# Kernel optimization log

Measured on AMD Instinct MI355X. Metric: run time of the kernel, lower is better.

Reference implementation:

```python
import jax, jax.numpy as jnp
import numpy as np

N_NODES = 50000
N_EDGES = 800000
D_IN, D_HID, D_OUT = 128, 256, 128


def _glorot(key, shape):
    fan_in, fan_out = shape[1], shape[0]
    lim = (6.0 / (fan_in + fan_out)) ** 0.5
    return jax.random.uniform(key, shape, jnp.float32, -lim, lim)


def setup_inputs() -> dict:
    key = jax.random.key(0)
    ks = jax.random.split(key, 8)
    x = jax.random.normal(ks[0], (N_NODES, D_IN), dtype=jnp.float32)
    edge_index = jax.random.randint(ks[1], (2, N_EDGES), 0, N_NODES, dtype=jnp.int64)
    # Layer 1: SAGEConv(D_IN -> D_HID); Layer 2: SAGEConv(D_HID -> D_OUT)
    # PyG SAGEConv: out = lin_l(mean_aggr(x_j)) + lin_r(x); bias lives in lin_l.
    Wl1 = _glorot(ks[2], (D_HID, D_IN))
    bl1 = jnp.zeros((D_HID,), jnp.float32)
    Wr1 = _glorot(ks[3], (D_HID, D_IN))
    Wl2 = _glorot(ks[4], (D_OUT, D_HID))
    bl2 = jnp.zeros((D_OUT,), jnp.float32)
    Wr2 = _glorot(ks[5], (D_OUT, D_HID))
    return {"x": x, "Wl1": Wl1, "bl1": bl1, "Wr1": Wr1,
            "Wl2": Wl2, "bl2": bl2, "Wr2": Wr2, "edge_index": edge_index}


def _sage_conv(x, src, dst, deg_inv, Wl, bl, Wr):
    # gather source features per edge, sum into dst buckets, normalize by in-degree
    msg_sum = jax.ops.segment_sum(x[src], dst, num_segments=N_NODES)  # [N, d_in]
    mean = msg_sum * deg_inv  # mean aggregation; isolated nodes -> zeros
    return mean @ Wl.T + bl + x @ Wr.T


def reference(x, Wl1, bl1, Wr1, Wl2, bl2, Wr2, edge_index):
    src, dst = edge_index[0], edge_index[1]
    deg = jax.ops.segment_sum(jnp.ones((N_EDGES,), jnp.float32), dst,
                              num_segments=N_NODES)
    deg_inv = (1.0 / jnp.maximum(deg, 1.0))[:, None]  # [N, 1]
    h = _sage_conv(x, src, dst, deg_inv, Wl1, bl1, Wr1)
    h = jax.nn.relu(h)  # dropout is identity in eval mode
    out = _sage_conv(h, src, dst, deg_inv, Wl2, bl2, Wr2)
    return out
```

## Files before the change

### kernel.cpp

```cpp
#include <hip/hip_runtime.h>
#include <hip/hip_fp16.h>

#define N_NODES 50000
#define N_EDGES 800000
#define D_IN 128
#define D_HID 256
#define D_OUT 128
#define NCHUNK 196
#define GEMM_GRID 512

typedef _Float16 f16x8 __attribute__((ext_vector_type(8)));
typedef float f32x4 __attribute__((ext_vector_type(4)));


__global__ void zero_deg(int* __restrict__ deg) {
    int i = blockIdx.x * blockDim.x + threadIdx.x;
    if (i < N_NODES) deg[i] = 0;
}

__global__ void deg_rank_kernel(const int* __restrict__ dst, int* __restrict__ deg,
                                int* __restrict__ rank) {
    int i = blockIdx.x * blockDim.x + threadIdx.x;
    if (i < N_EDGES) rank[i] = atomicAdd(&deg[dst[i]], 1);
}

__global__ void chunk_sum(const int* __restrict__ deg, int* __restrict__ partial) {
    __shared__ int s[256];
    int i = blockIdx.x * 256 + threadIdx.x;
    s[threadIdx.x] = (i < N_NODES) ? deg[i] : 0;
    __syncthreads();
    for (int off = 128; off > 0; off >>= 1) {
        if (threadIdx.x < off) s[threadIdx.x] += s[threadIdx.x + off];
        __syncthreads();
    }
    if (threadIdx.x == 0) partial[blockIdx.x] = s[0];
}

__global__ void chunk_scan(const int* __restrict__ partial, int* __restrict__ chunkOff) {
    __shared__ int s[256];
    int tid = threadIdx.x;
    int v = (tid < NCHUNK) ? partial[tid] : 0;
    s[tid] = v;
    __syncthreads();
    for (int off = 1; off < 256; off <<= 1) {
        int t = (tid >= off) ? s[tid - off] : 0;
        __syncthreads();
        s[tid] += t;
        __syncthreads();
    }
    if (tid < NCHUNK) chunkOff[tid] = s[tid] - v;
}

__global__ void scatter_scan(const int* __restrict__ deg, const int* __restrict__ chunkOff,
                             int* __restrict__ row_ptr, float* __restrict__ deg_inv) {
    __shared__ int s[256];
    int tid = threadIdx.x;
    int i = blockIdx.x * 256 + tid;
    int v = (i < N_NODES) ? deg[i] : 0;
    s[tid] = v;
    __syncthreads();
    for (int off = 1; off < 256; off <<= 1) {
        int t = (tid >= off) ? s[tid - off] : 0;
        __syncthreads();
        s[tid] += t;
        __syncthreads();
    }
    if (i < N_NODES) {
        int rp = chunkOff[blockIdx.x] + s[tid] - v;
        row_ptr[i] = rp;
        deg_inv[i] = 1.0f / fmaxf((float)v, 1.0f);
        if (i == N_NODES - 1) row_ptr[N_NODES] = N_EDGES;
    }
}

__global__ void fill_csr(const int* __restrict__ src, const int* __restrict__ dst,
                         const int* __restrict__ rank, const int* __restrict__ row_ptr,
                         int* __restrict__ csr_src) {
    int e = blockIdx.x * blockDim.x + threadIdx.x;
    if (e < N_EDGES) {
        csr_src[row_ptr[dst[e]] + rank[e]] = src[e];
    }
}


__global__ void cvt_half(const float* __restrict__ in, __half2* __restrict__ out, int n2) {
    int i = blockIdx.x * blockDim.x + threadIdx.x;
    if (i < n2) {
        float2 v = ((const float2*)in)[i];
        out[i] = __float22half2_rn(v);
    }
}

__global__ void cvt_weights(const float* __restrict__ a, const float* __restrict__ b,
                            const float* __restrict__ c, const float* __restrict__ d,
                            __half2* __restrict__ oa, __half2* __restrict__ ob,
                            __half2* __restrict__ oc, __half2* __restrict__ od) {
    int i = blockIdx.x * 256 + threadIdx.x;
    if (i < 16384) {
        oa[i] = __float22half2_rn(((const float2*)a)[i]);
        ob[i] = __float22half2_rn(((const float2*)b)[i]);
        oc[i] = __float22half2_rn(((const float2*)c)[i]);
        od[i] = __float22half2_rn(((const float2*)d)[i]);
    }
}


__global__ __launch_bounds__(256)
void gather_mean_h(const __half2* __restrict__ feat, const int* __restrict__ row_ptr,
                   const int* __restrict__ csr_src, const float* __restrict__ deg_inv,
                   __half2* __restrict__ outv) {
    const int lane = threadIdx.x & 63;
    const int n = blockIdx.x * 4 + (threadIdx.x >> 6);
    const int beg = row_ptr[n];
    const int end = row_ptr[n + 1];
    float a0 = 0.f, a1 = 0.f;
    int e = beg;
    for (; e + 8 <= end; e += 8) {
        int s0 = csr_src[e + 0], s1 = csr_src[e + 1];
        int s2 = csr_src[e + 2], s3 = csr_src[e + 3];
        int s4 = csr_src[e + 4], s5 = csr_src[e + 5];
        int s6 = csr_src[e + 6], s7 = csr_src[e + 7];
        float2 v0 = __half22float2(feat[s0 * 64 + lane]);
        float2 v1 = __half22float2(feat[s1 * 64 + lane]);
        float2 v2 = __half22float2(feat[s2 * 64 + lane]);
        float2 v3 = __half22float2(feat[s3 * 64 + lane]);
        float2 v4 = __half22float2(feat[s4 * 64 + lane]);
        float2 v5 = __half22float2(feat[s5 * 64 + lane]);
        float2 v6 = __half22float2(feat[s6 * 64 + lane]);
        float2 v7 = __half22float2(feat[s7 * 64 + lane]);
        a0 += ((v0.x + v1.x) + (v2.x + v3.x)) + ((v4.x + v5.x) + (v6.x + v7.x));
        a1 += ((v0.y + v1.y) + (v2.y + v3.y)) + ((v4.y + v5.y) + (v6.y + v7.y));
    }
    for (; e + 4 <= end; e += 4) {
        int s0 = csr_src[e + 0], s1 = csr_src[e + 1];
        int s2 = csr_src[e + 2], s3 = csr_src[e + 3];
        float2 v0 = __half22float2(feat[s0 * 64 + lane]);
        float2 v1 = __half22float2(feat[s1 * 64 + lane]);
        float2 v2 = __half22float2(feat[s2 * 64 + lane]);
        float2 v3 = __half22float2(feat[s3 * 64 + lane]);
        a0 += (v0.x + v1.x) + (v2.x + v3.x);
        a1 += (v0.y + v1.y) + (v2.y + v3.y);
    }
    for (; e < end; ++e) {
        float2 v = __half22float2(feat[csr_src[e] * 64 + lane]);
        a0 += v.x;
        a1 += v.y;
    }
    float di = deg_inv[n];
    outv[n * 64 + lane] = __float22half2_rn(make_float2(a0 * di, a1 * di));
}

__global__ __launch_bounds__(256)
void gather_mean_add_f32(const __half2* __restrict__ feat, const int* __restrict__ row_ptr,
                         const int* __restrict__ csr_src, const float* __restrict__ deg_inv,
                         float* __restrict__ out) {
    const int lane = threadIdx.x & 63;
    const int n = blockIdx.x * 4 + (threadIdx.x >> 6);
    const int beg = row_ptr[n];
    const int end = row_ptr[n + 1];
    float a0 = 0.f, a1 = 0.f;
    int e = beg;
    for (; e + 8 <= end; e += 8) {
        int s0 = csr_src[e + 0], s1 = csr_src[e + 1];
        int s2 = csr_src[e + 2], s3 = csr_src[e + 3];
        int s4 = csr_src[e + 4], s5 = csr_src[e + 5];
        int s6 = csr_src[e + 6], s7 = csr_src[e + 7];
        float2 v0 = __half22float2(feat[s0 * 64 + lane]);
        float2 v1 = __half22float2(feat[s1 * 64 + lane]);
        float2 v2 = __half22float2(feat[s2 * 64 + lane]);
        float2 v3 = __half22float2(feat[s3 * 64 + lane]);
        float2 v4 = __half22float2(feat[s4 * 64 + lane]);
        float2 v5 = __half22float2(feat[s5 * 64 + lane]);
        float2 v6 = __half22float2(feat[s6 * 64 + lane]);
        float2 v7 = __half22float2(feat[s7 * 64 + lane]);
        a0 += ((v0.x + v1.x) + (v2.x + v3.x)) + ((v4.x + v5.x) + (v6.x + v7.x));
        a1 += ((v0.y + v1.y) + (v2.y + v3.y)) + ((v4.y + v5.y) + (v6.y + v7.y));
    }
    for (; e + 4 <= end; e += 4) {
        int s0 = csr_src[e + 0], s1 = csr_src[e + 1];
        int s2 = csr_src[e + 2], s3 = csr_src[e + 3];
        float2 v0 = __half22float2(feat[s0 * 64 + lane]);
        float2 v1 = __half22float2(feat[s1 * 64 + lane]);
        float2 v2 = __half22float2(feat[s2 * 64 + lane]);
        float2 v3 = __half22float2(feat[s3 * 64 + lane]);
        a0 += (v0.x + v1.x) + (v2.x + v3.x);
        a1 += (v0.y + v1.y) + (v2.y + v3.y);
    }
    for (; e < end; ++e) {
        float2 v = __half22float2(feat[csr_src[e] * 64 + lane]);
        a0 += v.x;
        a1 += v.y;
    }
    float di = deg_inv[n];
    float2* o = (float2*)(out + (size_t)n * 128) + lane;
    float2 v = *o;
    v.x += a0 * di;
    v.y += a1 * di;
    *o = v;
}


__global__ __launch_bounds__(256, 2)
void gemm_l1(const __half* __restrict__ Aa, const __half* __restrict__ Ba,
             const __half* __restrict__ Ab, const __half* __restrict__ Bb,
             const float* __restrict__ bias, __half* __restrict__ H) {
    const int lane = threadIdx.x & 63;
    const int wave = threadIdx.x >> 6;
    const int quad = lane >> 4;
    const int l16 = lane & 15;
    const int koff = quad * 8;

    f16x8 bf[2][4][4];
    #pragma unroll
    for (int p = 0; p < 2; ++p) {
        const __half* __restrict__ B = p ? Bb : Ba;
        #pragma unroll
        for (int kc = 0; kc < 4; ++kc)
            #pragma unroll
            for (int nt = 0; nt < 4; ++nt)
                bf[p][kc][nt] = *(const f16x8*)(
                    B + (size_t)(wave * 64 + nt * 16 + l16) * D_IN + kc * 32 + koff);
    }
    float bv[4];
    #pragma unroll
    for (int nt = 0; nt < 4; ++nt) bv[nt] = bias[wave * 64 + nt * 16 + l16];

    const int NT = N_NODES / 16;
    const int g = gridDim.x;

    auto loadA = [&](int t, f16x8 (&a)[2][4]) {
        const size_t arow = (size_t)(t * 16 + l16) * D_IN + koff;
        #pragma unroll
        for (int kc = 0; kc < 4; ++kc) {
            a[0][kc] = *(const f16x8*)(Aa + arow + kc * 32);
            a[1][kc] = *(const f16x8*)(Ab + arow + kc * 32);
        }
    };
    auto step = [&](int tile, const f16x8 (&a)[2][4]) {
        f32x4 acc[4] = {};
        #pragma unroll
        for (int p = 0; p < 2; ++p)
            #pragma unroll
            for (int kc = 0; kc < 4; ++kc)
                #pragma unroll
                for (int nt = 0; nt < 4; ++nt)
                    acc[nt] = __builtin_amdgcn_mfma_f32_16x16x32_f16(
                        a[p][kc], bf[p][kc][nt], acc[nt], 0, 0, 0);
        #pragma unroll
        for (int nt = 0; nt < 4; ++nt) {
            int col = wave * 64 + nt * 16 + l16;
            #pragma unroll
            for (int r = 0; r < 4; ++r) {
                int row = tile * 16 + quad * 4 + r;
                H[(size_t)row * D_HID + col] =
                    __float2half(fmaxf(acc[nt][r] + bv[nt], 0.f));
            }
        }
    };

    f16x8 A0[2][4], A1[2][4];
    int tile = blockIdx.x;
    loadA(tile, A0);
    while (true) {
        if (tile + g < NT) loadA(tile + g, A1);
        step(tile, A0);
        tile += g;
        if (tile >= NT) break;
        if (tile + g < NT) loadA(tile + g, A0);
        step(tile, A1);
        tile += g;
        if (tile >= NT) break;
    }
}

__global__ __launch_bounds__(256, 2)
void gemm_l2(const __half* __restrict__ Hh, const __half* __restrict__ B0,
             const __half* __restrict__ B1, const float* __restrict__ bias,
             __half* __restrict__ P, float* __restrict__ out) {
    const int lane = threadIdx.x & 63;
    const int wave = threadIdx.x >> 6;
    const int quad = lane >> 4;
    const int l16 = lane & 15;
    const int koff = quad * 8;

    f16x8 bf0[8][2], bf1[8][2];
    #pragma unroll
    for (int kc = 0; kc < 8; ++kc)
        #pragma unroll
        for (int nt = 0; nt < 2; ++nt) {
            size_t brow = (size_t)(wave * 32 + nt * 16 + l16) * D_HID + kc * 32 + koff;
            bf0[kc][nt] = *(const f16x8*)(B0 + brow);
            bf1[kc][nt] = *(const f16x8*)(B1 + brow);
        }
    float bv[2];
    #pragma unroll
    for (int nt = 0; nt < 2; ++nt) bv[nt] = bias[wave * 32 + nt * 16 + l16];

    const int NT = N_NODES / 16;
    const int g = gridDim.x;

    auto loadA = [&](int t, f16x8 (&a)[8]) {
        const size_t arow = (size_t)(t * 16 + l16) * D_HID + koff;
        #pragma unroll
        for (int kc = 0; kc < 8; ++kc)
            a[kc] = *(const f16x8*)(Hh + arow + kc * 32);
    };
    auto step = [&](int tile, const f16x8 (&a)[8]) {
        f32x4 acc0[2] = {};
        f32x4 acc1[2] = {};
        #pragma unroll
        for (int kc = 0; kc < 8; ++kc)
            #pragma unroll
            for (int nt = 0; nt < 2; ++nt) {
                acc0[nt] = __builtin_amdgcn_mfma_f32_16x16x32_f16(
                    a[kc], bf0[kc][nt], acc0[nt], 0, 0, 0);
                acc1[nt] = __builtin_amdgcn_mfma_f32_16x16x32_f16(
                    a[kc], bf1[kc][nt], acc1[nt], 0, 0, 0);
            }
        #pragma unroll
        for (int nt = 0; nt < 2; ++nt) {
            int col = wave * 32 + nt * 16 + l16;
            #pragma unroll
            for (int r = 0; r < 4; ++r) {
                int row = tile * 16 + quad * 4 + r;
                P[(size_t)row * D_OUT + col] = __float2half(acc0[nt][r]);
                out[(size_t)row * D_OUT + col] = acc1[nt][r] + bv[nt];
            }
        }
    };

    f16x8 A0[8], A1[8];
    int tile = blockIdx.x;
    loadA(tile, A0);
    while (true) {
        if (tile + g < NT) loadA(tile + g, A1);
        step(tile, A0);
        tile += g;
        if (tile >= NT) break;
        if (tile + g < NT) loadA(tile + g, A0);
        step(tile, A1);
        tile += g;
        if (tile >= NT) break;
    }
}

extern "C" void kernel_launch(void* const* d_in, const int* in_sizes, int n_in,
                              void* d_out, int out_size, void* d_ws, size_t ws_size,
                              hipStream_t stream) {
    const float* x   = (const float*)d_in[0];
    const float* Wl1 = (const float*)d_in[1];
    const float* bl1 = (const float*)d_in[2];
    const float* Wr1 = (const float*)d_in[3];
    const float* Wl2 = (const float*)d_in[4];
    const float* bl2 = (const float*)d_in[5];
    const float* Wr2 = (const float*)d_in[6];
    const int*   ei  = (const int*)d_in[7];
    const int* src = ei;
    const int* dst = ei + N_EDGES;
    float* out = (float*)d_out;

    char* w = (char*)d_ws;
    auto alloc = [&](size_t bytes) {
        char* r = w;
        w += (bytes + 255) & ~(size_t)255;
        return r;
    };
    int*     deg       = (int*)alloc((size_t)N_NODES * 4);
    int*     row_ptr   = (int*)alloc((size_t)(N_NODES + 1) * 4);
    int*     rank      = (int*)alloc((size_t)N_EDGES * 4);
    int*     partial   = (int*)alloc(NCHUNK * 4);
    int*     chunkOff  = (int*)alloc(NCHUNK * 4);
    int*     csr_src   = (int*)alloc((size_t)N_EDGES * 4);
    float*   deg_inv   = (float*)alloc((size_t)N_NODES * 4);
    __half2* xb        = (__half2*)alloc((size_t)N_NODES * 64 * 4);
    __half2* mean1     = (__half2*)alloc((size_t)N_NODES * 64 * 4);
    __half*  h         = (__half*)alloc((size_t)N_NODES * 256 * 2);
    __half2* pb        = (__half2*)alloc((size_t)N_NODES * 64 * 4);
    __half*  wl1h      = (__half*)alloc(4 * 32768 * 2);
    __half*  wr1h = wl1h + 32768;
    __half*  wl2h = wr1h + 32768;
    __half*  wr2h = wl2h + 32768;

    zero_deg<<<(N_NODES + 255) / 256, 256, 0, stream>>>(deg);
    deg_rank_kernel<<<(N_EDGES + 255) / 256, 256, 0, stream>>>(dst, deg, rank);
    chunk_sum<<<NCHUNK, 256, 0, stream>>>(deg, partial);
    chunk_scan<<<1, 256, 0, stream>>>(partial, chunkOff);
    scatter_scan<<<NCHUNK, 256, 0, stream>>>(deg, chunkOff, row_ptr, deg_inv);
    fill_csr<<<(N_EDGES + 255) / 256, 256, 0, stream>>>(src, dst, rank, row_ptr, csr_src);

    cvt_half<<<12500, 256, 0, stream>>>(x, xb, N_NODES * 64);
    cvt_weights<<<64, 256, 0, stream>>>(Wl1, Wr1, Wl2, Wr2,
        (__half2*)wl1h, (__half2*)wr1h, (__half2*)wl2h, (__half2*)wr2h);

    gather_mean_h<<<12500, 256, 0, stream>>>(xb, row_ptr, csr_src, deg_inv, mean1);
    gemm_l1<<<GEMM_GRID, 256, 0, stream>>>(
        (const __half*)mean1, wl1h, (const __half*)xb, wr1h, bl1, h);

    gemm_l2<<<GEMM_GRID, 256, 0, stream>>>(
        h, wl2h, wr2h, bl2, (__half*)pb, out);
    gather_mean_add_f32<<<12500, 256, 0, stream>>>(pb, row_ptr, csr_src, deg_inv, out);
}
```

Before: 266.8 us.

## Gather neighbor rows with 16-byte loads, four edges per wave in parallel

Each wave is split into four 16-lane groups. Each group loads one full 128-half feature row with float4 loads, so four edges are processed per step instead of one row per wave via half2 loads. Partial sums are combined across groups with two xor shuffles, and group 0 writes the result with vector stores. This issues fewer, wider memory instructions and gives more independent rows in flight, at the cost of shuffle overhead and idle lanes on short tails.

```diff
diff --git a/kernel.cpp b/kernel.cpp
--- a/kernel.cpp
+++ b/kernel.cpp
@@ -105,98 +105,114 @@
 }
 
 
+__device__ __forceinline__ void accum_row4(const float4* __restrict__ feat4,
+                                           int src, int s, float (&acc)[8]) {
+    float4 v = feat4[(size_t)src * 16 + s];
+    const __half2* hp = (const __half2*)&v;
+    float2 f0 = __half22float2(hp[0]);
+    float2 f1 = __half22float2(hp[1]);
+    float2 f2 = __half22float2(hp[2]);
+    float2 f3 = __half22float2(hp[3]);
+    acc[0] += f0.x; acc[1] += f0.y;
+    acc[2] += f1.x; acc[3] += f1.y;
+    acc[4] += f2.x; acc[5] += f2.y;
+    acc[6] += f3.x; acc[7] += f3.y;
+}
+
 __global__ __launch_bounds__(256)
 void gather_mean_h(const __half2* __restrict__ feat, const int* __restrict__ row_ptr,
                    const int* __restrict__ csr_src, const float* __restrict__ deg_inv,
                    __half2* __restrict__ outv) {
+    const float4* feat4 = (const float4*)feat;
     const int lane = threadIdx.x & 63;
+    const int g = lane >> 4;
+    const int s = lane & 15;
     const int n = blockIdx.x * 4 + (threadIdx.x >> 6);
     const int beg = row_ptr[n];
     const int end = row_ptr[n + 1];
-    float a0 = 0.f, a1 = 0.f;
+    float acc[8] = {};
     int e = beg;
     for (; e + 8 <= end; e += 8) {
-        int s0 = csr_src[e + 0], s1 = csr_src[e + 1];
-        int s2 = csr_src[e + 2], s3 = csr_src[e + 3];
-        int s4 = csr_src[e + 4], s5 = csr_src[e + 5];
-        int s6 = csr_src[e + 6], s7 = csr_src[e + 7];
-        float2 v0 = __half22float2(feat[s0 * 64 + lane]);
-        float2 v1 = __half22float2(feat[s1 * 64 + lane]);
-        float2 v2 = __half22float2(feat[s2 * 64 + lane]);
-        float2 v3 = __half22float2(feat[s3 * 64 + lane]);
-        float2 v4 = __half22float2(feat[s4 * 64 + lane]);
-        float2 v5 = __half22float2(feat[s5 * 64 + lane]);
-        float2 v6 = __half22float2(feat[s6 * 64 + lane]);
-        float2 v7 = __half22float2(feat[s7 * 64 + lane]);
-        a0 += ((v0.x + v1.x) + (v2.x + v3.x)) + ((v4.x + v5.x) + (v6.x + v7.x));
-        a1 += ((v0.y + v1.y) + (v2.y + v3.y)) + ((v4.y + v5.y) + (v6.y + v7.y));
+        int s0 = csr_src[e + g];
+        int s1 = csr_src[e + 4 + g];
+        accum_row4(feat4, s0, s, acc);
+        accum_row4(feat4, s1, s, acc);
     }
     for (; e + 4 <= end; e += 4) {
-        int s0 = csr_src[e + 0], s1 = csr_src[e + 1];
-        int s2 = csr_src[e + 2], s3 = csr_src[e + 3];
-        float2 v0 = __half22float2(feat[s0 * 64 + lane]);
-        float2 v1 = __half22float2(feat[s1 * 64 + lane]);
-        float2 v2 = __half22float2(feat[s2 * 64 + lane]);
-        float2 v3 = __half22float2(feat[s3 * 64 + lane]);
-        a0 += (v0.x + v1.x) + (v2.x + v3.x);
-        a1 += (v0.y + v1.y) + (v2.y + v3.y);
-    }
-    for (; e < end; ++e) {
-        float2 v = __half22float2(feat[csr_src[e] * 64 + lane]);
-        a0 += v.x;
-        a1 += v.y;
-    }
-    float di = deg_inv[n];
-    outv[n * 64 + lane] = __float22half2_rn(make_float2(a0 * di, a1 * di));
+        int s0 = csr_src[e + g];
+        accum_row4(feat4, s0, s, acc);
+    }
+    if (e < end) {
+        int r = end - e;
+        if (g < r) {
+            int s0 = csr_src[e + g];
+            accum_row4(feat4, s0, s, acc);
+        }
+    }
+    #pragma unroll
+    for (int j = 0; j < 8; ++j) {
+        acc[j] += __shfl_xor(acc[j], 16);
+        acc[j] += __shfl_xor(acc[j], 32);
+    }
+    if (g == 0) {
+        float di = deg_inv[n];
+        float4 o;
+        __half2* op = (__half2*)&o;
+        op[0] = __float22half2_rn(make_float2(acc[0] * di, acc[1] * di));
+        op[1] = __float22half2_rn(make_float2(acc[2] * di, acc[3] * di));
+        op[2] = __float22half2_rn(make_float2(acc[4] * di, acc[5] * di));
+        op[3] = __float22half2_rn(make_float2(acc[6] * di, acc[7] * di));
+        ((float4*)(outv + (size_t)n * 64))[s] = o;
+    }
 }
 
 __global__ __launch_bounds__(256)
 void gather_mean_add_f32(const __half2* __restrict__ feat, const int* __restrict__ row_ptr,
                          const int* __restrict__ csr_src, const float* __restrict__ deg_inv,
                          float* __restrict__ out) {
+    const float4* feat4 = (const float4*)feat;
     const int lane = threadIdx.x & 63;
+    const int g = lane >> 4;
+    const int s = lane & 15;
     const int n = blockIdx.x * 4 + (threadIdx.x >> 6);
     const int beg = row_ptr[n];
     const int end = row_ptr[n + 1];
-    float a0 = 0.f, a1 = 0.f;
+    float acc[8] = {};
     int e = beg;
     for (; e + 8 <= end; e += 8) {
-        int s0 = csr_src[e + 0], s1 = csr_src[e + 1];
-        int s2 = csr_src[e + 2], s3 = csr_src[e + 3];
-        int s4 = csr_src[e + 4], s5 = csr_src[e + 5];
-        int s6 = csr_src[e + 6], s7 = csr_src[e + 7];
-        float2 v0 = __half22float2(feat[s0 * 64 + lane]);
-        float2 v1 = __half22float2(feat[s1 * 64 + lane]);
-        float2 v2 = __half22float2(feat[s2 * 64 + lane]);
-        float2 v3 = __half22float2(feat[s3 * 64 + lane]);
-        float2 v4 = __half22float2(feat[s4 * 64 + lane]);
-        float2 v5 = __half22float2(feat[s5 * 64 + lane]);
-        float2 v6 = __half22float2(feat[s6 * 64 + lane]);
-        float2 v7 = __half22float2(feat[s7 * 64 + lane]);
-        a0 += ((v0.x + v1.x) + (v2.x + v3.x)) + ((v4.x + v5.x) + (v6.x + v7.x));
-        a1 += ((v0.y + v1.y) + (v2.y + v3.y)) + ((v4.y + v5.y) + (v6.y + v7.y));
+        int s0 = csr_src[e + g];
+        int s1 = csr_src[e + 4 + g];
+        accum_row4(feat4, s0, s, acc);
+        accum_row4(feat4, s1, s, acc);
     }
     for (; e + 4 <= end; e += 4) {
-        int s0 = csr_src[e + 0], s1 = csr_src[e + 1];
-        int s2 = csr_src[e + 2], s3 = csr_src[e + 3];
-        float2 v0 = __half22float2(feat[s0 * 64 + lane]);
-        float2 v1 = __half22float2(feat[s1 * 64 + lane]);
-        float2 v2 = __half22float2(feat[s2 * 64 + lane]);
-        float2 v3 = __half22float2(feat[s3 * 64 + lane]);
-        a0 += (v0.x + v1.x) + (v2.x + v3.x);
-        a1 += (v0.y + v1.y) + (v2.y + v3.y);
-    }
-    for (; e < end; ++e) {
-        float2 v = __half22float2(feat[csr_src[e] * 64 + lane]);
-        a0 += v.x;
-        a1 += v.y;
-    }
-    float di = deg_inv[n];
-    float2* o = (float2*)(out + (size_t)n * 128) + lane;
-    float2 v = *o;
-    v.x += a0 * di;
-    v.y += a1 * di;
-    *o = v;
+        int s0 = csr_src[e + g];
+        accum_row4(feat4, s0, s, acc);
+    }
+    if (e < end) {
+        int r = end - e;
+        if (g < r) {
+            int s0 = csr_src[e + g];
+            accum_row4(feat4, s0, s, acc);
+        }
+    }
+    #pragma unroll
+    for (int j = 0; j < 8; ++j) {
+        acc[j] += __shfl_xor(acc[j], 16);
+        acc[j] += __shfl_xor(acc[j], 32);
+    }
+    if (g == 0) {
+        float di = deg_inv[n];
+        float4* orow = (float4*)(out + (size_t)n * 128);
+        float4 o0 = orow[s * 2];
+        float4 o1 = orow[s * 2 + 1];
+        o0.x += acc[0] * di; o0.y += acc[1] * di;
+        o0.z += acc[2] * di; o0.w += acc[3] * di;
+        o1.x += acc[4] * di; o1.y += acc[5] * di;
+        o1.z += acc[6] * di; o1.w += acc[7] * di;
+        orow[s * 2] = o0;
+        orow[s * 2 + 1] = o1;
+    }
 }
 
 
```

Result: no change. 263.5 us (-1.2%).
